# Performance work log

Hardware: AMD Instinct MI355X
Metric: run time of the kernel (lower is better)

## Reference

```python
import jax, jax.numpy as jnp
import numpy as np

DIM = 4096
NUM_HEAD = 32
NUM_KV_HEAD = 8
ROPE_THETA = 10000.0
B, T = 2, 2048


def apply_rope(x, start_pos=0, theta=ROPE_THETA):
    # x: [B, T, H, d_head]; rotate half-split pairs by position-dependent angles
    d = x.shape[-1]
    half = d // 2
    inv_freq = 1.0 / (theta ** (jnp.arange(0, half, dtype=jnp.float32) / half))
    pos = jnp.arange(x.shape[1], dtype=jnp.float32) + start_pos  # [T]
    ang = pos[:, None] * inv_freq[None, :]                       # [T, half]
    cos = jnp.cos(ang)[None, :, None, :]
    sin = jnp.sin(ang)[None, :, None, :]
    x1, x2 = x[..., :half], x[..., half:]
    return jnp.concatenate([x1 * cos - x2 * sin, x1 * sin + x2 * cos], axis=-1)


def setup_inputs() -> dict:
    key = jax.random.key(0)
    ks = jax.random.split(key, 5)
    scale = 0.02
    X = jax.random.normal(ks[0], (B, T, DIM), dtype=jnp.float32)
    Wq = jax.random.normal(ks[1], (DIM, DIM), dtype=jnp.float32) * scale
    Wk = jax.random.normal(ks[2], (DIM, DIM // NUM_HEAD * NUM_KV_HEAD), dtype=jnp.float32) * scale
    Wv = jax.random.normal(ks[3], (DIM, DIM // NUM_HEAD * NUM_KV_HEAD), dtype=jnp.float32) * scale
    Wo = jax.random.normal(ks[4], (DIM, DIM), dtype=jnp.float32) * scale
    return {"X": X, "Wq": Wq, "Wk": Wk, "Wv": Wv, "Wo": Wo}


def reference(X, Wq, Wk, Wv, Wo):
    Bs, Ts, C = X.shape
    H, Hkv = NUM_HEAD, NUM_KV_HEAD
    dh = C // H
    G = H // Hkv  # GQA group size

    Q = apply_rope((X @ Wq).reshape(Bs, Ts, H, dh))      # [B,T,H,dh]
    K = apply_rope((X @ Wk).reshape(Bs, Ts, Hkv, dh))    # [B,T,Hkv,dh]
    V = (X @ Wv).reshape(Bs, Ts, Hkv, dh)                # [B,T,Hkv,dh]

    # [B,Hkv,G,T,dh]: grouped layout equivalent to repeat_interleave on head dim
    Qh = Q.transpose(0, 2, 1, 3).reshape(Bs, Hkv, G, Ts, dh)
    Kh = K.transpose(0, 2, 1, 3)  # [B,Hkv,T,dh]
    Vh = V.transpose(0, 2, 1, 3)

    scores = jnp.einsum('bkgtd,bksd->bkgts', Qh, Kh) / jnp.sqrt(jnp.float32(dh))
    causal = jnp.tril(jnp.ones((Ts, Ts), dtype=bool))
    scores = jnp.where(causal[None, None, None], scores, -jnp.inf)
    attn = jax.nn.softmax(scores, axis=-1)
    out = jnp.einsum('bkgts,bksd->bkgtd', attn, Vh)       # [B,Hkv,G,T,dh]
    out = out.reshape(Bs, H, Ts, dh).transpose(0, 2, 1, 3).reshape(Bs, Ts, C)
    return out @ Wo
```

## Files before the change

kernel.cpp:

```cpp
#include <hip/hip_runtime.h>
#include <hip/hip_bf16.h>
#include <cstdint>
#include <cstddef>

#define B_   2
#define T_   2048
#define DIM_ 4096
#define H_   32
#define HKV_ 8
#define DH_  128
#define MROWS (B_*T_)
#define QKV_LD 6144

typedef __bf16 bf16_t;
typedef bf16_t bf16x8 __attribute__((ext_vector_type(8)));
typedef bf16_t bf16x4 __attribute__((ext_vector_type(4)));
typedef float  f32x4  __attribute__((ext_vector_type(4)));

typedef __attribute__((address_space(1))) void gvoid_t;
typedef __attribute__((address_space(3))) void lvoid_t;

__device__ __forceinline__ void gld_lds16(const void* g, void* l) {
  __builtin_amdgcn_global_load_lds((gvoid_t*)g, (lvoid_t*)l, 16, 0, 0);
}

__device__ __forceinline__ f32x4 mfma16(bf16x8 a, bf16x8 b, f32x4 c) {
  return __builtin_amdgcn_mfma_f32_16x16x32_bf16(a, b, c, 0, 0, 0);
}

__global__ void cast_f32_bf16(const float* __restrict__ in,
                              bf16_t* __restrict__ out, int n4) {
  int i = blockIdx.x * blockDim.x + threadIdx.x;
  if (i < n4) {
    float4 v = ((const float4*)in)[i];
    bf16x4 o;
    o[0] = (bf16_t)v.x; o[1] = (bf16_t)v.y; o[2] = (bf16_t)v.z; o[3] = (bf16_t)v.w;
    ((bf16x4*)out)[i] = o;
  }
}

__global__ void transpose_cast(const float* __restrict__ in,
                               bf16_t* __restrict__ out, int K, int N) {
  __shared__ float tile[32][33];
  int n0 = blockIdx.x * 32, k0 = blockIdx.y * 32;
  int tx = threadIdx.x, ty = threadIdx.y;
#pragma unroll
  for (int j = 0; j < 4; ++j)
    tile[ty + j*8][tx] = in[(size_t)(k0 + ty + j*8) * N + n0 + tx];
  __syncthreads();
#pragma unroll
  for (int j = 0; j < 4; ++j)
    out[(size_t)(n0 + ty + j*8) * K + k0 + tx] = (bf16_t)tile[tx][ty + j*8];
}

template <int OUT_F32>
__global__ __launch_bounds__(256, 2)
void gemm_bt(const bf16_t* __restrict__ A, const bf16_t* __restrict__ BT,
             void* __restrict__ C, int M, int N, int K) {
  __shared__ __align__(16) bf16_t Als[128 * 32];
  __shared__ __align__(16) bf16_t Bls[128 * 32];
  const int tid  = threadIdx.x;
  const int wave = tid >> 6, lane = tid & 63;
  const int quad = lane >> 4, l16 = lane & 15;
  const int wm = wave >> 1, wn = wave & 1;
  const int m0 = blockIdx.y * 128, n0 = blockIdx.x * 128;

  f32x4 acc[4][4] = {};

  const int srow = lane >> 2;
  const int scol = (lane & 3) * 8;

  for (int k0 = 0; k0 < K; k0 += 32) {
#pragma unroll
    for (int c = 0; c < 2; ++c) {
      int ch = wave * 2 + c;
      gld_lds16(A + (size_t)(m0 + ch*16 + srow) * K + k0 + scol,
                &Als[ch*512 + srow*32 + scol]);
    }
#pragma unroll
    for (int c = 0; c < 2; ++c) {
      int ch = wave * 2 + c;
      gld_lds16(BT + (size_t)(n0 + ch*16 + srow) * K + k0 + scol,
                &Bls[ch*512 + srow*32 + scol]);
    }
    __syncthreads();

    bf16x8 af[4], bfr[4];
#pragma unroll
    for (int mi = 0; mi < 4; ++mi)
      af[mi] = *(const bf16x8*)&Als[(wm*64 + mi*16 + l16)*32 + quad*8];
#pragma unroll
    for (int ni = 0; ni < 4; ++ni)
      bfr[ni] = *(const bf16x8*)&Bls[(wn*64 + ni*16 + l16)*32 + quad*8];
#pragma unroll
    for (int mi = 0; mi < 4; ++mi)
#pragma unroll
      for (int ni = 0; ni < 4; ++ni)
        acc[mi][ni] = mfma16(af[mi], bfr[ni], acc[mi][ni]);
    __syncthreads();
  }

#pragma unroll
  for (int mi = 0; mi < 4; ++mi)
#pragma unroll
    for (int ni = 0; ni < 4; ++ni)
#pragma unroll
      for (int r = 0; r < 4; ++r) {
        int row = m0 + wm*64 + mi*16 + quad*4 + r;
        int col = n0 + wn*64 + ni*16 + l16;
        if (OUT_F32)
          ((float*)C)[(size_t)row * N + col] = acc[mi][ni][r];
        else
          ((bf16_t*)C)[(size_t)row * N + col] = (bf16_t)acc[mi][ni][r];
      }
}

__global__ void rope_kernel(bf16_t* __restrict__ X, int Hn, int ld, int total) {
  int i = blockIdx.x * blockDim.x + threadIdx.x;
  if (i >= total) return;
  int d   = i & 63;
  int rem = i >> 6;
  int h   = rem % Hn; rem /= Hn;
  int t   = rem % T_;
  int b   = rem / T_;
  size_t base = (size_t)(b * T_ + t) * ld + h * DH_;
  float x1 = (float)X[base + d];
  float x2 = (float)X[base + 64 + d];
  float inv_freq = expf(-(float)d * 0.14391156758f);
  float ang = (float)t * inv_freq;
  float s, c;
  sincosf(ang, &s, &c);
  X[base + d]      = (bf16_t)(x1 * c - x2 * s);
  X[base + 64 + d] = (bf16_t)(x1 * s + x2 * c);
}

__global__ void v_transpose(const bf16_t* __restrict__ Vb,
                            bf16_t* __restrict__ VT, int ld) {
  __shared__ bf16_t tile[32][33];
  int t0 = blockIdx.x * 32;
  int d0 = blockIdx.y * 32;
  int bk = blockIdx.z;
  int b = bk >> 3, kv = bk & 7;
  int tx = threadIdx.x, ty = threadIdx.y;
#pragma unroll
  for (int j = 0; j < 4; ++j)
    tile[ty + j*8][tx] =
        Vb[(size_t)(b * T_ + t0 + ty + j*8) * ld + kv*DH_ + d0 + tx];
  __syncthreads();
#pragma unroll
  for (int j = 0; j < 4; ++j)
    VT[((size_t)bk * DH_ + d0 + ty + j*8) * T_ + t0 + tx] = tile[tx][ty + j*8];
}

__global__ __launch_bounds__(256, 2)
void flash_attn(const bf16_t* __restrict__ QKV, const bf16_t* __restrict__ VT,
                bf16_t* __restrict__ Ob) {
  __shared__ __align__(16) bf16_t Pls[128 * 72];

  const int tid = threadIdx.x, wave = tid >> 6, lane = tid & 63;
  const int quad = lane >> 4, l16 = lane & 15;

  const int linear = blockIdx.x;
  const int xcd  = linear & 7;
  const int slot = linear >> 3;
  const int g    = ((slot >> 6) << 3) + xcd;
  const int b    = g >> 3, kv = g & 7;
  const int j    = slot & 63;
  const int qt   = 15 - (j >> 2);
  const int h    = kv * 4 + (j & 3);

  bf16x8 q[2][4];
#pragma unroll
  for (int mi = 0; mi < 2; ++mi) {
    const bf16_t* base =
        QKV + (size_t)(b*T_ + qt*128 + wave*32 + mi*16 + l16) * QKV_LD + h*DH_;
#pragma unroll
    for (int kk = 0; kk < 4; ++kk)
      q[mi][kk] = *(const bf16x8*)(base + kk*32 + quad*8);
  }

  float m_st[2][4];
  f32x4 o_acc[2][8] = {};
  f32x4 l_acc[2] = {};
#pragma unroll
  for (int mi = 0; mi < 2; ++mi)
#pragma unroll
    for (int r = 0; r < 4; ++r) m_st[mi][r] = -1e30f;

  const int nkv = 2 * (qt + 1);
  const float S2 = 0.08838834764831845f * 1.4426950408889634f;
  const float THRraw = 8.0f / 0.08838834764831845f;

  const bf16_t* Kbase = QKV + DIM_ + (size_t)b * T_ * QKV_LD + kv * DH_;
  const bf16_t* Vbase = VT + (size_t)(b*HKV_ + kv) * DH_ * T_;

  bf16x8 vones;
#pragma unroll
  for (int i = 0; i < 8; ++i) vones[i] = (bf16_t)1.0f;

  for (int kvt = 0; kvt < nkv; ++kvt) {
    f32x4 s[2][4] = {};
#pragma unroll
    for (int kk = 0; kk < 4; ++kk) {
      bf16x8 kf[4];
#pragma unroll
      for (int ni = 0; ni < 4; ++ni) {
        int krow = kvt*64 + ni*16 + l16;
        kf[ni] = *(const bf16x8*)(Kbase + (size_t)krow * QKV_LD + kk*32 + quad*8);
      }
      __builtin_amdgcn_s_setprio(1);
#pragma unroll
      for (int mi = 0; mi < 2; ++mi)
#pragma unroll
        for (int ni = 0; ni < 4; ++ni)
          s[mi][ni] = mfma16(q[mi][kk], kf[ni], s[mi][ni]);
      __builtin_amdgcn_s_setprio(0);
    }

    const bool need_mask = (kvt >= 2*qt);
#pragma unroll
    for (int mi = 0; mi < 2; ++mi) {
      float lmax[4];
#pragma unroll
      for (int r = 0; r < 4; ++r) {
        int rpos = qt*128 + wave*32 + mi*16 + quad*4 + r;
        float m = -1e30f;
#pragma unroll
        for (int ni = 0; ni < 4; ++ni) {
          float v = s[mi][ni][r];
          if (need_mask) {
            int cpos = kvt*64 + ni*16 + l16;
            if (cpos > rpos) v = -1e30f;
          }
          s[mi][ni][r] = v;
          m = fmaxf(m, v);
        }
        lmax[r] = m;
      }
      bool defer = (lmax[0] <= m_st[mi][0] + THRraw) &
                   (lmax[1] <= m_st[mi][1] + THRraw) &
                   (lmax[2] <= m_st[mi][2] + THRraw) &
                   (lmax[3] <= m_st[mi][3] + THRraw);
      if (!__all(defer)) {
        float al[4];
#pragma unroll
        for (int r = 0; r < 4; ++r) {
          float m = lmax[r];
#pragma unroll
          for (int off = 1; off < 16; off <<= 1)
            m = fmaxf(m, __shfl_xor(m, off, 64));
          float mnew = fmaxf(m_st[mi][r], m);
          al[r] = __builtin_amdgcn_exp2f((m_st[mi][r] - mnew) * S2);
          m_st[mi][r] = mnew;
        }
#pragma unroll
        for (int ni = 0; ni < 8; ++ni)
#pragma unroll
          for (int r = 0; r < 4; ++r) o_acc[mi][ni][r] *= al[r];
#pragma unroll
        for (int r = 0; r < 4; ++r) l_acc[mi][r] *= al[r];
      }
#pragma unroll
      for (int r = 0; r < 4; ++r) {
        float mn2 = m_st[mi][r] * S2;
        int prow = wave*32 + mi*16 + quad*4 + r;
#pragma unroll
        for (int ni = 0; ni < 4; ++ni) {
          float pv = __builtin_amdgcn_exp2f(fmaf(s[mi][ni][r], S2, -mn2));
          Pls[prow*72 + ni*16 + l16] = (bf16_t)pv;
        }
      }
    }

    bf16x8 pf[2][2];
#pragma unroll
    for (int kk = 0; kk < 2; ++kk)
#pragma unroll
      for (int mi = 0; mi < 2; ++mi)
        pf[kk][mi] = *(const bf16x8*)&Pls[(wave*32 + mi*16 + l16)*72 + kk*32 + quad*8];

    __builtin_amdgcn_s_setprio(1);
    l_acc[0] = mfma16(pf[0][0], vones, l_acc[0]);
    l_acc[1] = mfma16(pf[0][1], vones, l_acc[1]);
    l_acc[0] = mfma16(pf[1][0], vones, l_acc[0]);
    l_acc[1] = mfma16(pf[1][1], vones, l_acc[1]);
    __builtin_amdgcn_s_setprio(0);

#pragma unroll
    for (int ni = 0; ni < 8; ++ni) {
      int drow = ni*16 + l16;
      const bf16_t* vb = Vbase + (size_t)drow * T_ + kvt*64;
      bf16x8 va = *(const bf16x8*)(vb + quad*8);
      bf16x8 vc = *(const bf16x8*)(vb + 32 + quad*8);
      __builtin_amdgcn_s_setprio(1);
      o_acc[0][ni] = mfma16(pf[0][0], va, o_acc[0][ni]);
      o_acc[1][ni] = mfma16(pf[0][1], va, o_acc[1][ni]);
      o_acc[0][ni] = mfma16(pf[1][0], vc, o_acc[0][ni]);
      o_acc[1][ni] = mfma16(pf[1][1], vc, o_acc[1][ni]);
      __builtin_amdgcn_s_setprio(0);
    }
  }

#pragma unroll
  for (int mi = 0; mi < 2; ++mi) {
    float inv[4];
#pragma unroll
    for (int r = 0; r < 4; ++r) inv[r] = 1.f / l_acc[mi][r];
#pragma unroll
    for (int ni = 0; ni < 8; ++ni)
#pragma unroll
      for (int r = 0; r < 4; ++r) {
        size_t row = (size_t)(b*T_ + qt*128 + wave*32 + mi*16 + quad*4 + r);
        int col = h*DH_ + ni*16 + l16;
        Ob[row * DIM_ + col] = (bf16_t)(o_acc[mi][ni][r] * inv[r]);
      }
  }
}

extern "C" void kernel_launch(void* const* d_in, const int* in_sizes, int n_in,
                              void* d_out, int out_size, void* d_ws, size_t ws_size,
                              hipStream_t stream) {
  const float* X  = (const float*)d_in[0];
  const float* Wq = (const float*)d_in[1];
  const float* Wk = (const float*)d_in[2];
  const float* Wv = (const float*)d_in[3];
  const float* Wo = (const float*)d_in[4];
  float* out = (float*)d_out;

  char* ws = (char*)d_ws;
  const size_t SZ_X   = (size_t)MROWS * DIM_ * 2;
  const size_t SZ_WQ  = (size_t)DIM_ * DIM_ * 2;
  const size_t SZ_WK  = (size_t)DIM_ * 1024 * 2;
  const size_t SZ_QKV = (size_t)MROWS * QKV_LD * 2;
  bf16_t* Xb  = (bf16_t*)(ws);
  bf16_t* WqT = (bf16_t*)(ws + SZ_X);
  bf16_t* WkT = (bf16_t*)(ws + SZ_X + SZ_WQ);
  bf16_t* WvT = (bf16_t*)(ws + SZ_X + SZ_WQ + SZ_WK);
  bf16_t* WoT = (bf16_t*)(ws + SZ_X + SZ_WQ + 2*SZ_WK);
  bf16_t* QKV = (bf16_t*)(ws + SZ_X + 2*SZ_WQ + 2*SZ_WK);
  bf16_t* VT  = (bf16_t*)(ws + SZ_X + 2*SZ_WQ + 2*SZ_WK + SZ_QKV);
  bf16_t* Ob  = Xb;

  {
    int n4 = MROWS * DIM_ / 4;
    cast_f32_bf16<<<(n4 + 255)/256, 256, 0, stream>>>(X, Xb, n4);
  }
  transpose_cast<<<dim3(DIM_/32, DIM_/32), dim3(32,8), 0, stream>>>(Wq, WqT, DIM_, DIM_);
  transpose_cast<<<dim3(1024/32, DIM_/32), dim3(32,8), 0, stream>>>(Wk, WkT, DIM_, 1024);
  transpose_cast<<<dim3(1024/32, DIM_/32), dim3(32,8), 0, stream>>>(Wv, WvT, DIM_, 1024);
  transpose_cast<<<dim3(DIM_/32, DIM_/32), dim3(32,8), 0, stream>>>(Wo, WoT, DIM_, DIM_);

  gemm_bt<0><<<dim3(QKV_LD/128, MROWS/128), 256, 0, stream>>>(Xb, WqT, QKV, MROWS, QKV_LD, DIM_);

  {
    int totq = B_ * T_ * H_ * 64;
    rope_kernel<<<(totq + 255)/256, 256, 0, stream>>>(QKV, H_, QKV_LD, totq);
    int totk = B_ * T_ * HKV_ * 64;
    rope_kernel<<<(totk + 255)/256, 256, 0, stream>>>(QKV + DIM_, HKV_, QKV_LD, totk);
  }

  v_transpose<<<dim3(T_/32, DH_/32, B_*HKV_), dim3(32,8), 0, stream>>>(QKV + DIM_ + 1024, VT, QKV_LD);

  flash_attn<<<dim3((T_/128) * H_ * B_), 256, 0, stream>>>(QKV, VT, Ob);

  gemm_bt<1><<<dim3(DIM_/128, MROWS/128), 256, 0, stream>>>(Ob, WoT, out, MROWS, DIM_, DIM_);
}
```

Baseline: 901.3 us.

## Split long causal query tiles across two blocks and merge partials

Query tiles 8-15 now have their KV range split into two halves, each handled by its own block. Each half writes unnormalized fp32 partial outputs plus row max and sum into scratch space that reuses the output buffer and the WqT buffer. A new combine kernel merges the halves with log-sum-exp weights and writes bf16 output. A hand-written work-item order interleaves long and short items to balance load across the grid. The cost is extra fp32 partial traffic and one more kernel launch.

```diff
diff --git a/kernel.cpp b/kernel.cpp
--- a/kernel.cpp
+++ b/kernel.cpp
@@ -152,22 +152,31 @@
     VT[((size_t)bk * DH_ + d0 + ty + j*8) * T_ + t0 + tx] = tile[tx][ty + j*8];
 }
 
+static __device__ const signed char it_qt[24] =
+  {7,15,15,14,14, 6,13,13,12,12, 5,11,11,10,10, 4, 9, 9, 8, 8, 3, 2, 1, 0};
+static __device__ const signed char it_hf[24] =
+  {0, 0, 1, 0, 1, 0, 0, 1, 0, 1, 0, 0, 1, 0, 1, 0, 0, 1, 0, 1, 0, 0, 0, 0};
+
 __global__ __launch_bounds__(256, 2)
 void flash_attn(const bf16_t* __restrict__ QKV, const bf16_t* __restrict__ VT,
-                bf16_t* __restrict__ Ob) {
+                bf16_t* __restrict__ Ob, float* __restrict__ Part,
+                float* __restrict__ Mbuf, float* __restrict__ Lbuf) {
   __shared__ __align__(16) bf16_t Pls[128 * 72];
 
   const int tid = threadIdx.x, wave = tid >> 6, lane = tid & 63;
   const int quad = lane >> 4, l16 = lane & 15;
 
-  const int linear = blockIdx.x;
-  const int xcd  = linear & 7;
-  const int slot = linear >> 3;
-  const int g    = ((slot >> 6) << 3) + xcd;
-  const int b    = g >> 3, kv = g & 7;
-  const int j    = slot & 63;
-  const int qt   = 15 - (j >> 2);
-  const int h    = kv * 4 + (j & 3);
+  const int id   = blockIdx.x;
+  const int w    = id & 63;
+  const int item = id >> 6;
+  const int qt   = it_qt[item];
+  const int half = it_hf[item];
+  const bool isB = (qt >= 8);
+  const int kv = w & 7, b = (w >> 3) & 1;
+  const int h  = kv * 4 + (w >> 4);
+
+  const int cnt = isB ? (qt + 1) : 2 * (qt + 1);
+  const int kv0 = isB ? half * (qt + 1) : 0;
 
   bf16x8 q[2][4];
 #pragma unroll
@@ -187,7 +196,6 @@
 #pragma unroll
     for (int r = 0; r < 4; ++r) m_st[mi][r] = -1e30f;
 
-  const int nkv = 2 * (qt + 1);
   const float S2 = 0.08838834764831845f * 1.4426950408889634f;
   const float THRraw = 8.0f / 0.08838834764831845f;
 
@@ -198,7 +206,7 @@
 #pragma unroll
   for (int i = 0; i < 8; ++i) vones[i] = (bf16_t)1.0f;
 
-  for (int kvt = 0; kvt < nkv; ++kvt) {
+  for (int kvt = kv0; kvt < kv0 + cnt; ++kvt) {
     f32x4 s[2][4] = {};
 #pragma unroll
     for (int kk = 0; kk < 4; ++kk) {
@@ -301,19 +309,87 @@
     }
   }
 
-#pragma unroll
-  for (int mi = 0; mi < 2; ++mi) {
-    float inv[4];
-#pragma unroll
-    for (int r = 0; r < 4; ++r) inv[r] = 1.f / l_acc[mi][r];
-#pragma unroll
-    for (int ni = 0; ni < 8; ++ni)
-#pragma unroll
-      for (int r = 0; r < 4; ++r) {
-        size_t row = (size_t)(b*T_ + qt*128 + wave*32 + mi*16 + quad*4 + r);
-        int col = h*DH_ + ni*16 + l16;
-        Ob[row * DIM_ + col] = (bf16_t)(o_acc[mi][ni][r] * inv[r]);
-      }
+  if (!isB) {
+#pragma unroll
+    for (int mi = 0; mi < 2; ++mi) {
+      float inv[4];
+#pragma unroll
+      for (int r = 0; r < 4; ++r) inv[r] = 1.f / l_acc[mi][r];
+#pragma unroll
+      for (int ni = 0; ni < 8; ++ni)
+#pragma unroll
+        for (int r = 0; r < 4; ++r) {
+          size_t row = (size_t)(b*T_ + qt*128 + wave*32 + mi*16 + quad*4 + r);
+          int col = h*DH_ + ni*16 + l16;
+          Ob[row * DIM_ + col] = (bf16_t)(o_acc[mi][ni][r] * inv[r]);
+        }
+    }
+  } else {
+    const int i16 = (qt - 8) * 2 + half;
+    float* pb = Part + ((size_t)(i16 * 64 + w)) * 128 * 128;
+#pragma unroll
+    for (int mi = 0; mi < 2; ++mi)
+#pragma unroll
+      for (int ni = 0; ni < 8; ++ni)
+#pragma unroll
+        for (int r = 0; r < 4; ++r) {
+          int row = wave*32 + mi*16 + quad*4 + r;
+          int col = ni*16 + l16;
+          pb[row*128 + col] = o_acc[mi][ni][r];
+        }
+    if (l16 == 0) {
+      const int sb = (i16 * 64 + w) * 128;
+#pragma unroll
+      for (int mi = 0; mi < 2; ++mi)
+#pragma unroll
+        for (int r = 0; r < 4; ++r) {
+          int row = wave*32 + mi*16 + quad*4 + r;
+          Mbuf[sb + row] = m_st[mi][r];
+          Lbuf[sb + row] = l_acc[mi][r];
+        }
+    }
+  }
+}
+
+__global__ void combine_attn(const float* __restrict__ Part,
+                             const float* __restrict__ Mbuf,
+                             const float* __restrict__ Lbuf,
+                             bf16_t* __restrict__ Ob) {
+  const int bid = blockIdx.x;
+  const int qtb = bid >> 6;
+  const int w   = bid & 63;
+  const int kv = w & 7, b = (w >> 3) & 1;
+  const int h  = kv * 4 + (w >> 4);
+  const int qt = 8 + qtb;
+  const int tid = threadIdx.x;
+  const int r  = tid >> 1;
+  const int ch = (tid & 1) * 64;
+
+  const int i0 = qtb * 2, i1 = qtb * 2 + 1;
+  const float m0 = Mbuf[(i0*64 + w)*128 + r];
+  const float m1 = Mbuf[(i1*64 + w)*128 + r];
+  const float l0 = Lbuf[(i0*64 + w)*128 + r];
+  const float l1 = Lbuf[(i1*64 + w)*128 + r];
+  const float mx = fmaxf(m0, m1);
+  const float S2 = 0.08838834764831845f * 1.4426950408889634f;
+  const float w0 = __builtin_amdgcn_exp2f((m0 - mx) * S2);
+  const float w1 = __builtin_amdgcn_exp2f((m1 - mx) * S2);
+  const float inv = 1.f / (w0 * l0 + w1 * l1);
+
+  const float* p0 = Part + ((size_t)(i0*64 + w))*128*128 + (size_t)r*128 + ch;
+  const float* p1 = Part + ((size_t)(i1*64 + w))*128*128 + (size_t)r*128 + ch;
+  bf16_t* op = Ob + (size_t)(b*T_ + qt*128 + r) * DIM_ + h*DH_ + ch;
+
+#pragma unroll
+  for (int c = 0; c < 64; c += 4) {
+    float4 a = *(const float4*)(p0 + c);
+    float4 d = *(const float4*)(p1 + c);
+    bf16x4 o;
+    o[0] = (bf16_t)((a.x * w0 + d.x * w1) * inv);
+    o[1] = (bf16_t)((a.y * w0 + d.y * w1) * inv);
+    o[2] = (bf16_t)((a.z * w0 + d.z * w1) * inv);
+    o[3] = (bf16_t)((a.w * w0 + d.w * w1) * inv);
+    *(bf16x4*)(op + c) = o;
   }
 }
 
@@ -341,6 +417,10 @@
   bf16_t* VT  = (bf16_t*)(ws + SZ_X + 2*SZ_WQ + 2*SZ_WK + SZ_QKV);
   bf16_t* Ob  = Xb;
 
+  float* Part = out;
+  float* Mbuf = (float*)WqT;
+  float* Lbuf = Mbuf + 16*64*128;
+
   {
     int n4 = MROWS * DIM_ / 4;
     cast_f32_bf16<<<(n4 + 255)/256, 256, 0, stream>>>(X, Xb, n4);
@@ -361,7 +441,9 @@
 
   v_transpose<<<dim3(T_/32, DH_/32, B_*HKV_), dim3(32,8), 0, stream>>>(QKV + DIM_ + 1024, VT, QKV_LD);
 
-  flash_attn<<<dim3((T_/128) * H_ * B_), 256, 0, stream>>>(QKV, VT, Ob);
+  flash_attn<<<dim3(24 * 64), 256, 0, stream>>>(QKV, VT, Ob, Part, Mbuf, Lbuf);
+
+  combine_attn<<<dim3(8 * 64), 256, 0, stream>>>(Part, Mbuf, Lbuf, Ob);
 
   gemm_bt<1><<<dim3(DIM_/128, MROWS/128), 256, 0, stream>>>(Ob, WoT, out, MROWS, DIM_, DIM_);
 }
```

Result: slower. 956.3 us (+6.1%).

## Shrink flash attention query tile to 64 rows and raise occupancy

Applied to the files above, without the earlier changes.

The flash attention kernel now handles 64 query rows per block (16 per wave) instead of 128, halving registers and LDS per block and raising launch bounds to 4 blocks per CU. The grid doubles to 2048 blocks and the block-to-head mapping is rewritten, dropping the XCD-aware grouping in favour of a simple ordering with the largest query blocks first. This aims to improve latency hiding and load balance across the causal triangle, at the cost of loading each K/V tile from global memory twice as often per query row and losing the explicit XCD L2 locality.

```diff
diff --git a/kernel.cpp b/kernel.cpp
--- a/kernel.cpp
+++ b/kernel.cpp
@@ -152,42 +152,36 @@
     VT[((size_t)bk * DH_ + d0 + ty + j*8) * T_ + t0 + tx] = tile[tx][ty + j*8];
 }
 
-__global__ __launch_bounds__(256, 2)
+__global__ __launch_bounds__(256, 4)
 void flash_attn(const bf16_t* __restrict__ QKV, const bf16_t* __restrict__ VT,
                 bf16_t* __restrict__ Ob) {
-  __shared__ __align__(16) bf16_t Pls[128 * 72];
+  __shared__ __align__(16) bf16_t Pls[64 * 72];
 
   const int tid = threadIdx.x, wave = tid >> 6, lane = tid & 63;
   const int quad = lane >> 4, l16 = lane & 15;
 
-  const int linear = blockIdx.x;
-  const int xcd  = linear & 7;
-  const int slot = linear >> 3;
-  const int g    = ((slot >> 6) << 3) + xcd;
-  const int b    = g >> 3, kv = g & 7;
-  const int j    = slot & 63;
-  const int qt   = 15 - (j >> 2);
-  const int h    = kv * 4 + (j & 3);
-
-  bf16x8 q[2][4];
-#pragma unroll
-  for (int mi = 0; mi < 2; ++mi) {
+  const int id = blockIdx.x;
+  const int w  = id & 63;
+  const int qb = 31 - (id >> 6);
+  const int kv = w & 7, b = (w >> 3) & 1;
+  const int h  = kv * 4 + (w >> 4);
+
+  bf16x8 q[4];
+  {
     const bf16_t* base =
-        QKV + (size_t)(b*T_ + qt*128 + wave*32 + mi*16 + l16) * QKV_LD + h*DH_;
+        QKV + (size_t)(b*T_ + qb*64 + wave*16 + l16) * QKV_LD + h*DH_;
 #pragma unroll
     for (int kk = 0; kk < 4; ++kk)
-      q[mi][kk] = *(const bf16x8*)(base + kk*32 + quad*8);
-  }
-
-  float m_st[2][4];
-  f32x4 o_acc[2][8] = {};
-  f32x4 l_acc[2] = {};
-#pragma unroll
-  for (int mi = 0; mi < 2; ++mi)
-#pragma unroll
-    for (int r = 0; r < 4; ++r) m_st[mi][r] = -1e30f;
-
-  const int nkv = 2 * (qt + 1);
+      q[kk] = *(const bf16x8*)(base + kk*32 + quad*8);
+  }
+
+  float m_st[4];
+  f32x4 o_acc[8] = {};
+  f32x4 l_acc = {};
+#pragma unroll
+  for (int r = 0; r < 4; ++r) m_st[r] = -1e30f;
+
+  const int nkv = qb + 1;
   const float S2 = 0.08838834764831845f * 1.4426950408889634f;
   const float THRraw = 8.0f / 0.08838834764831845f;
 
@@ -199,7 +193,7 @@
   for (int i = 0; i < 8; ++i) vones[i] = (bf16_t)1.0f;
 
   for (int kvt = 0; kvt < nkv; ++kvt) {
-    f32x4 s[2][4] = {};
+    f32x4 s[4] = {};
 #pragma unroll
     for (int kk = 0; kk < 4; ++kk) {
       bf16x8 kf[4];
@@ -210,80 +204,71 @@
       }
       __builtin_amdgcn_s_setprio(1);
 #pragma unroll
-      for (int mi = 0; mi < 2; ++mi)
-#pragma unroll
-        for (int ni = 0; ni < 4; ++ni)
-          s[mi][ni] = mfma16(q[mi][kk], kf[ni], s[mi][ni]);
+      for (int ni = 0; ni < 4; ++ni)
+        s[ni] = mfma16(q[kk], kf[ni], s[ni]);
       __builtin_amdgcn_s_setprio(0);
     }
 
-    const bool need_mask = (kvt >= 2*qt);
-#pragma unroll
-    for (int mi = 0; mi < 2; ++mi) {
-      float lmax[4];
+    const bool need_mask = (kvt == qb);
+    float lmax[4];
+#pragma unroll
+    for (int r = 0; r < 4; ++r) {
+      int rpos = qb*64 + wave*16 + quad*4 + r;
+      float m = -1e30f;
+#pragma unroll
+      for (int ni = 0; ni < 4; ++ni) {
+        float v = s[ni][r];
+        if (need_mask) {
+          int cpos = kvt*64 + ni*16 + l16;
+          if (cpos > rpos) v = -1e30f;
+        }
+        s[ni][r] = v;
+        m = fmaxf(m, v);
+      }
+      lmax[r] = m;
+    }
+    bool defer = (lmax[0] <= m_st[0] + THRraw) &
+                 (lmax[1] <= m_st[1] + THRraw) &
+                 (lmax[2] <= m_st[2] + THRraw) &
+                 (lmax[3] <= m_st[3] + THRraw);
+    if (!__all(defer)) {
+      float al[4];
 #pragma unroll
       for (int r = 0; r < 4; ++r) {
-        int rpos = qt*128 + wave*32 + mi*16 + quad*4 + r;
-        float m = -1e30f;
-#pragma unroll
-        for (int ni = 0; ni < 4; ++ni) {
-          float v = s[mi][ni][r];
-          if (need_mask) {
-            int cpos = kvt*64 + ni*16 + l16;
-            if (cpos > rpos) v = -1e30f;
-          }
-          s[mi][ni][r] = v;
-          m = fmaxf(m, v);
-        }
-        lmax[r] = m;
-      }
-      bool defer = (lmax[0] <= m_st[mi][0] + THRraw) &
-                   (lmax[1] <= m_st[mi][1] + THRraw) &
-                   (lmax[2] <= m_st[mi][2] + THRraw) &
-                   (lmax[3] <= m_st[mi][3] + THRraw);
-      if (!__all(defer)) {
-        float al[4];
-#pragma unroll
-        for (int r = 0; r < 4; ++r) {
-          float m = lmax[r];
-#pragma unroll
-          for (int off = 1; off < 16; off <<= 1)
-            m = fmaxf(m, __shfl_xor(m, off, 64));
-          float mnew = fmaxf(m_st[mi][r], m);
-          al[r] = __builtin_amdgcn_exp2f((m_st[mi][r] - mnew) * S2);
-          m_st[mi][r] = mnew;
-        }
-#pragma unroll
-        for (int ni = 0; ni < 8; ++ni)
-#pragma unroll
-          for (int r = 0; r < 4; ++r) o_acc[mi][ni][r] *= al[r];
-#pragma unroll
-        for (int r = 0; r < 4; ++r) l_acc[mi][r] *= al[r];
-      }
-#pragma unroll
-      for (int r = 0; r < 4; ++r) {
-        float mn2 = m_st[mi][r] * S2;
-        int prow = wave*32 + mi*16 + quad*4 + r;
-#pragma unroll
-        for (int ni = 0; ni < 4; ++ni) {
-          float pv = __builtin_amdgcn_exp2f(fmaf(s[mi][ni][r], S2, -mn2));
-          Pls[prow*72 + ni*16 + l16] = (bf16_t)pv;
-        }
-      }
-    }
-
-    bf16x8 pf[2][2];
+        float m = lmax[r];
+#pragma unroll
+        for (int off = 1; off < 16; off <<= 1)
+          m = fmaxf(m, __shfl_xor(m, off, 64));
+        float mnew = fmaxf(m_st[r], m);
+        al[r] = __builtin_amdgcn_exp2f((m_st[r] - mnew) * S2);
+        m_st[r] = mnew;
+      }
+#pragma unroll
+      for (int ni = 0; ni < 8; ++ni)
+#pragma unroll
+        for (int r = 0; r < 4; ++r) o_acc[ni][r] *= al[r];
+#pragma unroll
+      for (int r = 0; r < 4; ++r) l_acc[r] *= al[r];
+    }
+#pragma unroll
+    for (int r = 0; r < 4; ++r) {
+      float mn2 = m_st[r] * S2;
+      int prow = wave*16 + quad*4 + r;
+#pragma unroll
+      for (int ni = 0; ni < 4; ++ni) {
+        float pv = __builtin_amdgcn_exp2f(fmaf(s[ni][r], S2, -mn2));
+        Pls[prow*72 + ni*16 + l16] = (bf16_t)pv;
+      }
+    }
+
+    bf16x8 pf[2];
 #pragma unroll
     for (int kk = 0; kk < 2; ++kk)
-#pragma unroll
-      for (int mi = 0; mi < 2; ++mi)
-        pf[kk][mi] = *(const bf16x8*)&Pls[(wave*32 + mi*16 + l16)*72 + kk*32 + quad*8];
+      pf[kk] = *(const bf16x8*)&Pls[(wave*16 + l16)*72 + kk*32 + quad*8];
 
     __builtin_amdgcn_s_setprio(1);
-    l_acc[0] = mfma16(pf[0][0], vones, l_acc[0]);
-    l_acc[1] = mfma16(pf[0][1], vones, l_acc[1]);
-    l_acc[0] = mfma16(pf[1][0], vones, l_acc[0]);
-    l_acc[1] = mfma16(pf[1][1], vones, l_acc[1]);
+    l_acc = mfma16(pf[0], vones, l_acc);
+    l_acc = mfma16(pf[1], vones, l_acc);
     __builtin_amdgcn_s_setprio(0);
 
 #pragma unroll
@@ -293,26 +278,23 @@
       bf16x8 va = *(const bf16x8*)(vb + quad*8);
       bf16x8 vc = *(const bf16x8*)(vb + 32 + quad*8);
       __builtin_amdgcn_s_setprio(1);
-      o_acc[0][ni] = mfma16(pf[0][0], va, o_acc[0][ni]);
-      o_acc[1][ni] = mfma16(pf[0][1], va, o_acc[1][ni]);
-      o_acc[0][ni] = mfma16(pf[1][0], vc, o_acc[0][ni]);
-      o_acc[1][ni] = mfma16(pf[1][1], vc, o_acc[1][ni]);
+      o_acc[ni] = mfma16(pf[0], va, o_acc[ni]);
+      o_acc[ni] = mfma16(pf[1], vc, o_acc[ni]);
       __builtin_amdgcn_s_setprio(0);
     }
   }
 
-#pragma unroll
-  for (int mi = 0; mi < 2; ++mi) {
+  {
     float inv[4];
 #pragma unroll
-    for (int r = 0; r < 4; ++r) inv[r] = 1.f / l_acc[mi][r];
+    for (int r = 0; r < 4; ++r) inv[r] = 1.f / l_acc[r];
 #pragma unroll
     for (int ni = 0; ni < 8; ++ni)
 #pragma unroll
       for (int r = 0; r < 4; ++r) {
-        size_t row = (size_t)(b*T_ + qt*128 + wave*32 + mi*16 + quad*4 + r);
+        size_t row = (size_t)(b*T_ + qb*64 + wave*16 + quad*4 + r);
         int col = h*DH_ + ni*16 + l16;
-        Ob[row * DIM_ + col] = (bf16_t)(o_acc[mi][ni][r] * inv[r]);
+        Ob[row * DIM_ + col] = (bf16_t)(o_acc[ni][r] * inv[r]);
       }
   }
 }
@@ -361,7 +343,7 @@
 
   v_transpose<<<dim3(T_/32, DH_/32, B_*HKV_), dim3(32,8), 0, stream>>>(QKV + DIM_ + 1024, VT, QKV_LD);
 
-  flash_attn<<<dim3((T_/128) * H_ * B_), 256, 0, stream>>>(QKV, VT, Ob);
+  flash_attn<<<dim3(32 * 64), 256, 0, stream>>>(QKV, VT, Ob);
 
   gemm_bt<1><<<dim3(DIM_/128, MROWS/128), 256, 0, stream>>>(Ob, WoT, out, MROWS, DIM_, DIM_);
 }
```

Measured after the change: 1.127 ms. +25.0%, slower.
